# Kernel tuning notes

Measured on AMD Instinct MI355X. Metric: run time of the kernel, lower is better.

Reference implementation:

```python
import jax, jax.numpy as jnp
import numpy as np

B, M, N, D, H = 2, 10, 1024, 128, 8
HD = D // H  # head_dim = 16


def setup_inputs() -> dict:
    key = jax.random.key(0)
    ks = jax.random.split(key, 10)
    s = 0.02
    return {
        "node_emb": jax.random.normal(ks[0], (B, N, D), jnp.float32),
        "prefer_emb": jax.random.normal(ks[1], (B, M, N, D), jnp.float32),
        "Wqkv_w": jax.random.normal(ks[2], (D, 3 * D), jnp.float32) * s,
        "Wqkv_b": jnp.zeros((3 * D,), jnp.float32),
        "wq_p_w": jax.random.normal(ks[3], (D, D), jnp.float32) * s,
        "wq_p_b": jnp.zeros((D,), jnp.float32),
        "wk_p_w": jax.random.normal(ks[4], (D, D), jnp.float32) * s,
        "wk_p_b": jnp.zeros((D,), jnp.float32),
        "out_w": jax.random.normal(ks[5], (D, D), jnp.float32) * s,
        "out_b": jnp.zeros((D,), jnp.float32),
    }


def reference(node_emb, prefer_emb, Wqkv_w, Wqkv_b, wq_p_w, wq_p_b, wk_p_w, wk_p_b, out_w, out_b):
    # qkv projection: (b, n, 3d) -> q, k, v each (b, n, d)
    qkv = node_emb @ Wqkv_w + Wqkv_b
    q, k, v = jnp.split(qkv, 3, axis=-1)
    # preference-conditioned q/k: (b, m, n, d)
    pq = prefer_emb @ wq_p_w + wq_p_b
    pk = prefer_emb @ wk_p_w + wk_p_b
    q5 = q[:, None, :, :] + pq  # (b, m, n, d)
    k5 = k[:, None, :, :] + pk
    # split heads: (b, m, n, d) -> (b, h, m, n, hd)
    def heads(x):
        return x.reshape(B, M, N, H, HD).transpose(0, 3, 1, 2, 4)
    qh, kh = heads(q5), heads(k5)
    vh = v.reshape(B, N, H, HD).transpose(0, 2, 1, 3)  # (b, h, n, hd)
    # scores: (b, h, m, n_q, n_k), scaled by sqrt(head_dim)
    scores = jnp.einsum('bhmqd,bhmkd->bhmqk', qh, kh) / jnp.sqrt(jnp.asarray(HD, jnp.float32))
    # softmax over the preference dim m, then sum over m -> (b, h, n_q, n_k)
    attn = jax.nn.softmax(scores, axis=2).sum(axis=2)
    out = jnp.einsum('bhqk,bhkd->bhqd', attn, vh)  # (b, h, n, hd)
    out = out.transpose(0, 2, 1, 3).reshape(B, N, D)
    return out @ out_w + out_b
```

## Files before the change

### kernel.cpp

```cpp
#include <hip/hip_runtime.h>


#define NN 1024
#define DD 128
#define TRIPLE (3 * DD)

__global__ void k_colsum(const float* __restrict__ node,
                         float* __restrict__ partial) {
    int bk = blockIdx.x;
    int t = threadIdx.x;
    int f4col = t & 31;
    int rowsub = t >> 5;
    const float4* base = (const float4*)node;
    size_t row0 = (size_t)bk * 32 + rowsub;
    float4 acc = make_float4(0.f, 0.f, 0.f, 0.f);
#pragma unroll
    for (int it = 0; it < 4; ++it) {
        float4 v = base[(row0 + it * 8) * 32 + f4col];
        acc.x += v.x; acc.y += v.y; acc.z += v.z; acc.w += v.w;
    }
    __shared__ float4 s_red[256];
    s_red[t] = acc;
    __syncthreads();
    if (t < 32) {
        float4 a = s_red[t];
#pragma unroll
        for (int j = 1; j < 8; ++j) {
            float4 v = s_red[t + 32 * j];
            a.x += v.x; a.y += v.y; a.z += v.z; a.w += v.w;
        }
        ((float4*)partial)[bk * 32 + t] = a;
    }
}

__global__ void k_fused(const float* __restrict__ partial,
                        const float* __restrict__ Wqkv_w,
                        const float* __restrict__ Wqkv_b,
                        const float* __restrict__ out_w,
                        const float* __restrict__ out_b,
                        float4* __restrict__ out4) {
    __shared__ float s_ne[256];
    __shared__ float s_vs[256];
    __shared__ float s_row[256];
    int t = threadIdx.x;
    int b = t >> 7;
    int d = t & (DD - 1);

    float ne = 0.f;
#pragma unroll 8
    for (int p = 0; p < 32; ++p)
        ne += partial[((b << 5) + p) * DD + d];
    s_ne[t] = ne;
    __syncthreads();

    float acc = Wqkv_b[2 * DD + d] * (float)NN;
#pragma unroll 8
    for (int c = 0; c < DD; ++c)
        acc += s_ne[(b << 7) + c] * Wqkv_w[c * TRIPLE + 2 * DD + d];
    s_vs[t] = acc;
    __syncthreads();

    float r = out_b[d];
#pragma unroll 8
    for (int c = 0; c < DD; ++c)
        r += s_vs[(b << 7) + c] * out_w[c * DD + d];
    s_row[t] = r;
    __syncthreads();

    int gi = blockIdx.x * 256 + t;
    const float4* row4 = (const float4*)s_row;
    out4[gi] = row4[((gi >> 15) << 5) | (gi & 31)];
}

extern "C" void kernel_launch(void* const* d_in, const int* in_sizes, int n_in,
                              void* d_out, int out_size, void* d_ws, size_t ws_size,
                              hipStream_t stream) {
    const float* node   = (const float*)d_in[0];
    const float* Wqkv_w = (const float*)d_in[2];
    const float* Wqkv_b = (const float*)d_in[3];
    const float* out_w  = (const float*)d_in[8];
    const float* out_b  = (const float*)d_in[9];

    float* partial = (float*)d_ws;

    k_colsum<<<dim3(64), dim3(256), 0, stream>>>(node, partial);
    k_fused<<<dim3(256), dim3(256), 0, stream>>>(partial, Wqkv_w, Wqkv_b,
                                                 out_w, out_b, (float4*)d_out);
}
```

Before: 17.58 us.

## Fuse column-sum and projection kernels into one launch with a flag grid barrier

Merges the column-sum kernel and the fused projection kernel into a single 64-block kernel. The blocks synchronise through per-block flag words in workspace, using release and acquire fences and a spin-wait. Each block then writes four times as many output float4s. The aim is to remove the second kernel launch and the gap between launches. The flags are never reset, so on repeated calls the barrier can pass before the current call's partial sums are written. That is a correctness risk unless the workspace is cleared between calls.

```diff
diff --git a/kernel.cpp b/kernel.cpp
--- a/kernel.cpp
+++ b/kernel.cpp
@@ -4,47 +4,64 @@
 #define NN 1024
 #define DD 128
 #define TRIPLE (3 * DD)
+#define NBLK 64
+#define MAGIC 0x5EEDF00Du
 
-__global__ void k_colsum(const float* __restrict__ node,
-                         float* __restrict__ partial) {
-    int bk = blockIdx.x;
-    int t = threadIdx.x;
-    int f4col = t & 31;
-    int rowsub = t >> 5;
-    const float4* base = (const float4*)node;
-    size_t row0 = (size_t)bk * 32 + rowsub;
-    float4 acc = make_float4(0.f, 0.f, 0.f, 0.f);
+__global__ void __launch_bounds__(256)
+k_all(const float* __restrict__ node,
+      const float* __restrict__ Wqkv_w,
+      const float* __restrict__ Wqkv_b,
+      const float* __restrict__ out_w,
+      const float* __restrict__ out_b,
+      float4* __restrict__ out4,
+      float* __restrict__ partial,
+      unsigned* __restrict__ magic) {
+    const int bk = blockIdx.x;
+    const int t  = threadIdx.x;
+
+    {
+        const int f4col  = t & 31;
+        const int rowsub = t >> 5;
+        const float4* base = (const float4*)node;
+        const size_t row0 = (size_t)bk * 32 + rowsub;
+        float4 acc = make_float4(0.f, 0.f, 0.f, 0.f);
 #pragma unroll
-    for (int it = 0; it < 4; ++it) {
-        float4 v = base[(row0 + it * 8) * 32 + f4col];
-        acc.x += v.x; acc.y += v.y; acc.z += v.z; acc.w += v.w;
+        for (int it = 0; it < 4; ++it) {
+            float4 v = base[(row0 + (size_t)it * 8) * 32 + f4col];
+            acc.x += v.x; acc.y += v.y; acc.z += v.z; acc.w += v.w;
+        }
+        __shared__ float4 s_red[256];
+        s_red[t] = acc;
+        __syncthreads();
+        if (t < 32) {
+            float4 a = s_red[t];
+#pragma unroll
+            for (int j = 1; j < 8; ++j) {
+                float4 v = s_red[t + 32 * j];
+                a.x += v.x; a.y += v.y; a.z += v.z; a.w += v.w;
+            }
+            ((float4*)partial)[bk * 32 + t] = a;
+        }
     }
-    __shared__ float4 s_red[256];
-    s_red[t] = acc;
+    __builtin_amdgcn_fence(__ATOMIC_RELEASE, "agent");
     __syncthreads();
-    if (t < 32) {
-        float4 a = s_red[t];
-#pragma unroll
-        for (int j = 1; j < 8; ++j) {
-            float4 v = s_red[t + 32 * j];
-            a.x += v.x; a.y += v.y; a.z += v.z; a.w += v.w;
-        }
-        ((float4*)partial)[bk * 32 + t] = a;
+    if (t == 0)
+        __hip_atomic_store(&magic[bk], MAGIC, __ATOMIC_RELAXED,
+                           __HIP_MEMORY_SCOPE_AGENT);
+
+    if (t < NBLK) {
+        while (__hip_atomic_load(&magic[t], __ATOMIC_RELAXED,
+                                 __HIP_MEMORY_SCOPE_AGENT) != MAGIC)
+            __builtin_amdgcn_s_sleep(1);
     }
-}
+    __syncthreads();
+    __builtin_amdgcn_fence(__ATOMIC_ACQUIRE, "agent");
 
-__global__ void k_fused(const float* __restrict__ partial,
-                        const float* __restrict__ Wqkv_w,
-                        const float* __restrict__ Wqkv_b,
-                        const float* __restrict__ out_w,
-                        const float* __restrict__ out_b,
-                        float4* __restrict__ out4) {
     __shared__ float s_ne[256];
     __shared__ float s_vs[256];
     __shared__ float s_row[256];
-    int t = threadIdx.x;
-    int b = t >> 7;
-    int d = t & (DD - 1);
+    const int b = t >> 7;
+    const int d = t & (DD - 1);
 
     float ne = 0.f;
 #pragma unroll 8
@@ -67,9 +84,13 @@
     s_row[t] = r;
     __syncthreads();
 
-    int gi = blockIdx.x * 256 + t;
     const float4* row4 = (const float4*)s_row;
-    out4[gi] = row4[((gi >> 15) << 5) | (gi & 31)];
+    const int gbase = bk * 1024;
+#pragma unroll
+    for (int i = 0; i < 4; ++i) {
+        int gi = gbase + i * 256 + t;
+        out4[gi] = row4[((gi >> 15) << 5) | (gi & 31)];
+    }
 }
 
 extern "C" void kernel_launch(void* const* d_in, const int* in_sizes, int n_in,
@@ -81,9 +102,10 @@
     const float* out_w  = (const float*)d_in[8];
     const float* out_b  = (const float*)d_in[9];
 
-    float* partial = (float*)d_ws;
+    float*    partial = (float*)d_ws;
+    unsigned* magic   = (unsigned*)(partial + NBLK * DD);
 
-    k_colsum<<<dim3(64), dim3(256), 0, stream>>>(node, partial);
-    k_fused<<<dim3(256), dim3(256), 0, stream>>>(partial, Wqkv_w, Wqkv_b,
-                                                 out_w, out_b, (float4*)d_out);
+    k_all<<<dim3(NBLK), dim3(256), 0, stream>>>(node, Wqkv_w, Wqkv_b,
+                                                out_w, out_b,
+                                                (float4*)d_out, partial, magic);
 }
```

Result: slower. 18.61 us (+5.8%).
